# Kernel tuning notes

Measured on AMD Instinct MI355X. Metric: run time of the kernel, lower is better.

## Reference

```python
import jax, jax.numpy as jnp
import numpy as np

HEADS = 8
DIM_KEY = 32
DIM_VALUE = 32
SCALE = DIM_KEY ** -0.5
RED = 2  # reduction_factor


def _conv(x, w, stride):
    # NHWC input, HWIO kernel, VALID padding (keras Conv2D default)
    return jax.lax.conv_general_dilated(
        x, w, window_strides=(stride, stride), padding='VALID',
        dimension_numbers=('NHWC', 'HWIO', 'NHWC'))


def _split_heads(t, h):
    # [b, H, W, h*d] -> [b, h, H*W, d]
    b, H, W, hd = t.shape
    d = hd // h
    return t.reshape(b, H * W, h, d).transpose(0, 2, 1, 3)


def setup_inputs() -> dict:
    key = jax.random.key(0)
    ks = jax.random.split(key, 6)
    dim = 256
    x = jax.random.normal(ks[0], (8, 56, 56, dim), dtype=jnp.float32)
    Wq = jax.random.normal(ks[1], (1, 1, dim, DIM_KEY * HEADS), dtype=jnp.float32) * 0.02
    Wk = jax.random.normal(ks[2], (RED, RED, dim, DIM_KEY * HEADS), dtype=jnp.float32) * 0.02
    Wv = jax.random.normal(ks[3], (RED, RED, dim, DIM_VALUE * HEADS), dtype=jnp.float32) * 0.02
    Wo = jax.random.normal(ks[4], (1, 1, DIM_VALUE * HEADS, dim), dtype=jnp.float32) * 0.02
    bo = jnp.zeros((dim,), dtype=jnp.float32)
    return {"x": x, "Wq": Wq, "Wk": Wk, "Wv": Wv, "Wo": Wo, "bo": bo}


def reference(x, Wq, Wk, Wv, Wo, bo):
    b, H, W, _ = x.shape
    q = _split_heads(_conv(x, Wq, 1), HEADS)      # [b, h, H*W, dk]
    k = _split_heads(_conv(x, Wk, RED), HEADS)    # [b, h, (H/R)*(W/R), dk]
    v = _split_heads(_conv(x, Wv, RED), HEADS)    # [b, h, (H/R)*(W/R), dv]
    dots = jnp.einsum('bhnd,bhmd->bhnm', q, k) * SCALE
    attn = jax.nn.softmax(dots, axis=-1)
    out = jnp.einsum('bhnm,bhmd->bhnd', attn, v)  # [b, h, H*W, dv]
    out = out.transpose(0, 2, 1, 3).reshape(b, H, W, HEADS * DIM_VALUE)
    out = _conv(out, Wo, 1) + bo                  # 1x1 output projection (dropout rate 0)
    return out
```

## Files before the change

kernel.cpp:

```cpp
#include <hip/hip_runtime.h>
#include <cstdint>
#include <cstddef>

typedef __bf16 bf16_t;
typedef __bf16 bf16x8 __attribute__((ext_vector_type(8)));
typedef __bf16 bf16x4 __attribute__((ext_vector_type(4)));
typedef float  f32x4  __attribute__((ext_vector_type(4)));
typedef unsigned int u32x2 __attribute__((ext_vector_type(2)));
typedef unsigned int u32x4 __attribute__((ext_vector_type(4)));

#define MFMA16(a,b,c) __builtin_amdgcn_mfma_f32_16x16x32_bf16((a),(b),(c),0,0,0)

#if __has_builtin(__builtin_amdgcn_exp2f)
#define EXP2F(x) __builtin_amdgcn_exp2f(x)
#else
#define EXP2F(x) exp2f(x)
#endif

namespace {
constexpr int BATCH = 8;
constexpr int NQ    = 56 * 56;
constexpr int NKV   = 28 * 28;
constexpr int NKVP  = 800;
constexpr float QSCALE = 0.17677669529663687f * 1.44269504088896340f;

constexpr size_t XB_ELEMS = (size_t)BATCH * 56 * 56 * 256;
constexpr size_t Q_ELEMS  = (size_t)64 * NQ * 32;
constexpr size_t K_ELEMS  = (size_t)64 * NKVP * 32;
constexpr size_t VT_ELEMS = (size_t)64 * 32 * NKVP;

constexpr size_t XB_OFF  = 0;
constexpr size_t Q_OFF   = XB_OFF + XB_ELEMS * 2;
constexpr size_t K_OFF   = Q_OFF + Q_ELEMS * 2;
constexpr size_t VT_OFF  = K_OFF + K_ELEMS * 2;
constexpr size_t WQT_OFF = VT_OFF + VT_ELEMS * 2;
constexpr size_t WKT_OFF = WQT_OFF + (size_t)65536 * 2;
constexpr size_t WVT_OFF = WKT_OFF + (size_t)262144 * 2;
constexpr size_t WOT_OFF = WVT_OFF + (size_t)262144 * 2;
}

__device__ __forceinline__ void perm32swap(uint32_t& a, uint32_t& b) {
  asm volatile("s_nop 1\n\tv_permlane32_swap_b32 %0, %1\n\ts_nop 1"
               : "+v"(a), "+v"(b));
}


__global__ __launch_bounds__(256) void k_prep(const float* __restrict__ x,
                                              const float* __restrict__ Wq,
                                              const float* __restrict__ Wk,
                                              const float* __restrict__ Wv,
                                              const float* __restrict__ Wo,
                                              bf16_t* __restrict__ xb,
                                              bf16_t* __restrict__ Wqt,
                                              bf16_t* __restrict__ Wkt,
                                              bf16_t* __restrict__ Wvt,
                                              bf16_t* __restrict__ Wot,
                                              bf16_t* __restrict__ Kh,
                                              bf16_t* __restrict__ Vt) {
  const int bid = blockIdx.x;
  if (bid < 6272) {
    int i = bid * 256 + threadIdx.x;
    float4 v = ((const float4*)x)[i];
    bf16x4 o;
    o[0] = (bf16_t)v.x; o[1] = (bf16_t)v.y; o[2] = (bf16_t)v.z; o[3] = (bf16_t)v.w;
    ((bf16x4*)xb)[i] = o;
    return;
  }
  if (bid < 6432) {
    __shared__ float tile[64][65];
    const int wid = bid - 6272;
    const float* w; bf16_t* wt; int K; float scale = 1.f; int local;
    if (wid < 16)       { w = Wq; wt = Wqt; K = 256;  scale = QSCALE; local = wid; }
    else if (wid < 80)  { w = Wk; wt = Wkt; K = 1024; local = wid - 16; }
    else if (wid < 144) { w = Wv; wt = Wvt; K = 1024; local = wid - 80; }
    else                { w = Wo; wt = Wot; K = 256;  local = wid - 144; }
    const int tk = (local >> 2) * 64, tn = (local & 3) * 64;
    const int t = threadIdx.x;
#pragma unroll
    for (int i = 0; i < 16; ++i) {
      int e = t + i * 256, kk = e >> 6, nn = e & 63;
      tile[kk][nn] = w[(size_t)(tk + kk) * 256 + tn + nn];
    }
    __syncthreads();
#pragma unroll
    for (int i = 0; i < 16; ++i) {
      int e = t + i * 256, nn = e >> 6, kk = e & 63;
      wt[(size_t)(tn + nn) * K + tk + kk] = (bf16_t)(tile[kk][nn] * scale);
    }
    return;
  }
  const int pair = bid - 6432;
  bf16_t* kp = Kh + (size_t)pair * NKVP * 32 + (size_t)NKV * 32;
  for (int i = threadIdx.x; i < 512; i += 256) kp[i] = (bf16_t)0.f;
  bf16_t* vp = Vt + (size_t)pair * 32 * NKVP;
  for (int i = threadIdx.x; i < 512; i += 256) {
    int d = i >> 4, c = i & 15;
    vp[(size_t)d * NKVP + NKV + c] = (bf16_t)0.f;
  }
}


__global__ __launch_bounds__(512) void k_gemm_q(const bf16_t* __restrict__ A,
                                                const bf16_t* __restrict__ Wt,
                                                bf16_t* __restrict__ Qh) {
  __shared__ __align__(16) char Blds[64 * 512];
  const int t = threadIdx.x;
  const int lane = t & 63, wv = t >> 6;
  const int lq = lane & 15, grp = lane >> 4;
  const int w = (blockIdx.x & 7) * 98 + (blockIdx.x >> 3);
  const int m0 = (w >> 2) * 128 + wv * 16;
  const int n0 = (w & 3) * 64;

#pragma unroll
  for (int i = 0; i < 4; ++i) {
    int c = t + i * 512;
    int r = c >> 5, cb = (c & 31) << 4;
    bf16x8 v = *(const bf16x8*)(Wt + (size_t)(n0 + r) * 256 + (cb >> 1));
    *(bf16x8*)(Blds + r * 512 + (cb ^ ((r & 7) << 4))) = v;
  }
  __syncthreads();

  const bf16_t* Arow = A + (size_t)(m0 + lq) * 256 + grp * 8;
  f32x4 acc[4] = {};
#pragma unroll
  for (int kk = 0; kk < 8; ++kk) {
    bf16x8 af = *(const bf16x8*)(Arow + kk * 32);
#pragma unroll
    for (int nt = 0; nt < 4; ++nt) {
      const int r = nt * 16 + lq;
      bf16x8 bfr = *(const bf16x8*)(Blds + r * 512 + ((kk * 64 + grp * 16) ^ ((r & 7) << 4)));
      acc[nt] = MFMA16(af, bfr, acc[nt]);
    }
  }

  const int grow = m0 + grp * 4;
  const int b = grow / NQ, pos = grow - b * NQ;
#pragma unroll
  for (int nt = 0; nt < 4; ++nt) {
    const int n = n0 + nt * 16 + lq;
    const int h = n >> 5, d = n & 31;
    bf16_t* dst = Qh + ((size_t)(b * 8 + h) * NQ + pos) * 32 + d;
#pragma unroll
    for (int j = 0; j < 4; ++j) dst[(size_t)j * 32] = (bf16_t)acc[nt][j];
  }
}


__global__ __launch_bounds__(512) void k_gemm_kv(const bf16_t* __restrict__ xb,
                                                 const bf16_t* __restrict__ Wkt,
                                                 const bf16_t* __restrict__ Wvt,
                                                 bf16_t* __restrict__ Kh,
                                                 bf16_t* __restrict__ Vt) {
  __shared__ __align__(16) char Blds[64 * 1024];
  const int t = threadIdx.x;
  const int lane = t & 63, wv = t >> 6;
  const int lq = lane & 15, grp = lane >> 4;
  const int w = (blockIdx.x & 7) * 49 + (blockIdx.x >> 3);
  const int rem = w & 7;
  const int mode = rem & 1;
  const int n0 = (rem >> 1) * 64;
  const int mt = (w >> 3) * 128 + wv * 16;
  const bf16_t* Wt = mode ? Wvt : Wkt;

  const int grow = mt + lq;
  const int b = grow / NKV, pos = grow - b * NKV;
  const int pi = pos / 28, pj = pos % 28;
  const bf16_t* x4[4];
#pragma unroll
  for (int hw = 0; hw < 4; ++hw) {
    const int h_ = hw >> 1, w_ = hw & 1;
    x4[hw] = xb + ((size_t)((b * 56 + 2 * pi + h_) * 56) + 2 * pj + w_) * 256 + grp * 8;
  }

  f32x4 acc[4] = {};
#pragma unroll
  for (int half = 0; half < 2; ++half) {
    if (half) __syncthreads();
#pragma unroll
    for (int i = 0; i < 8; ++i) {
      int c = t + i * 512;
      int r = c >> 6, cb = (c & 63) << 4;
      bf16x8 v = *(const bf16x8*)(Wt + (size_t)(n0 + r) * 1024 + half * 512 + (cb >> 1));
      *(bf16x8*)(Blds + r * 1024 + (cb ^ ((r & 7) << 4))) = v;
    }
    __syncthreads();
#pragma unroll
    for (int kk = 0; kk < 16; ++kk) {
      const int gk = half * 16 + kk;
      const int hw = gk >> 3, kkk = gk & 7;
      bf16x8 af = *(const bf16x8*)(x4[hw] + kkk * 32);
#pragma unroll
      for (int nt = 0; nt < 4; ++nt) {
        const int r = nt * 16 + lq;
        bf16x8 bfr = *(const bf16x8*)(Blds + r * 1024 + ((kk * 64 + grp * 16) ^ ((r & 7) << 4)));
        acc[nt] = MFMA16(af, bfr, acc[nt]);
      }
    }
  }

  const int mbase = mt + grp * 4;
  const int b2 = mbase / NKV, pos2 = mbase - b2 * NKV;
  if (mode == 0) {
#pragma unroll
    for (int nt = 0; nt < 4; ++nt) {
      const int n = n0 + nt * 16 + lq;
      const int h = n >> 5, d = n & 31;
      bf16_t* dst = Kh + ((size_t)(b2 * 8 + h) * NKVP + pos2) * 32 + d;
#pragma unroll
      for (int j = 0; j < 4; ++j) dst[(size_t)j * 32] = (bf16_t)acc[nt][j];
    }
  } else {
#pragma unroll
    for (int nt = 0; nt < 4; ++nt) {
      const int n = n0 + nt * 16 + lq;
      const int h = n >> 5, d = n & 31;
      bf16x4 v;
#pragma unroll
      for (int j = 0; j < 4; ++j) v[j] = (bf16_t)acc[nt][j];
      *(bf16x4*)&Vt[((size_t)(b2 * 8 + h) * 32 + d) * NKVP + pos2] = v;
    }
  }
}


__global__ __launch_bounds__(256) void k_attn(const bf16_t* __restrict__ Qh,
                                              const bf16_t* __restrict__ Kh,
                                              const bf16_t* __restrict__ Vt,
                                              bf16_t* __restrict__ att) {
  const int lane = threadIdx.x & 63, wv = threadIdx.x >> 6;
  const int lq = lane & 15, grp = lane >> 4;
  const int wg = blockIdx.x;
  const int idx = wg >> 3;
  const int ygrp = (wg & 7) * 2 + idx / 98;
  const int pair = ygrp * 4 + wv;
  const int q0 = (idx % 98) * 32;

  const bf16_t* Qbase = Qh + ((size_t)pair * NQ + q0) * 32;
  bf16x8 qf[2];
#pragma unroll
  for (int t = 0; t < 2; ++t)
    qf[t] = *(const bf16x8*)(Qbase + (size_t)(t * 16 + lq) * 32 + grp * 8);

  const int prow = (lq & 3) | ((lq & 4) << 1) | ((lq & 8) >> 1);
  const bf16_t* Kb = Kh + (size_t)pair * NKVP * 32 + (size_t)prow * 32 + grp * 8;
  const bf16_t* Vb = Vt + (size_t)pair * 32 * NKVP + grp * 8;

  const f32x4 fz = {0.f, 0.f, 0.f, 0.f};
  f32x4 ps[2] = {fz, fz};
  f32x4 ot[2][2] = {{fz, fz}, {fz, fz}};

  bf16x8 Ak0, Ak1, Av0, Av1, Bk0, Bk1, Bv0, Bv1;

#define LOADF(P, CH) do { const int kv0_ = (CH) * 32;                          \
    P##k0 = *(const bf16x8*)(Kb + (size_t)kv0_ * 32);                          \
    P##k1 = *(const bf16x8*)(Kb + (size_t)(kv0_ + 16) * 32);                   \
    P##v0 = *(const bf16x8*)(Vb + (size_t)lq * NKVP + kv0_);                   \
    P##v1 = *(const bf16x8*)(Vb + (size_t)(16 + lq) * NKVP + kv0_); } while (0)

#define COMPUTE(P) do {                                                        \
    _Pragma("unroll")                                                          \
    for (int t = 0; t < 2; ++t) {                                              \
      f32x4 s0 = MFMA16(P##k0, qf[t], fz);                                     \
      f32x4 s1 = MFMA16(P##k1, qf[t], fz);                                     \
      f32x4 e0, e1;                                                            \
      _Pragma("unroll")                                                        \
      for (int j = 0; j < 4; ++j) { e0[j] = EXP2F(s0[j]); e1[j] = EXP2F(s1[j]); } \
      ps[t] += e0 + e1;                                                        \
      bf16x4 pa, pb;                                                           \
      _Pragma("unroll")                                                        \
      for (int j = 0; j < 4; ++j) { pa[j] = (bf16_t)e0[j]; pb[j] = (bf16_t)e1[j]; } \
      u32x2 ua = __builtin_bit_cast(u32x2, pa);                                \
      u32x2 ub = __builtin_bit_cast(u32x2, pb);                                \
      uint32_t x0 = ua[0], x1 = ua[1], y0 = ub[0], y1 = ub[1];                 \
      perm32swap(x0, y0);                                                      \
      perm32swap(x1, y1);                                                      \
      u32x4 pfu = {x0, x1, y0, y1};                                            \
      bf16x8 pf = __builtin_bit_cast(bf16x8, pfu);                             \
      ot[t][0] = MFMA16(P##v0, pf, ot[t][0]);                                  \
      ot[t][1] = MFMA16(P##v1, pf, ot[t][1]);                                  \
    } } while (0)

  LOADF(A, 0);
#pragma unroll 1
  for (int i = 0; i < 12; ++i) {
    LOADF(B, 2 * i + 1);
    COMPUTE(A);
    LOADF(A, 2 * i + 2);
    COMPUTE(B);
  }
  COMPUTE(A);
#undef LOADF
#undef COMPUTE

#pragma unroll
  for (int t = 0; t < 2; ++t) {
    float l = ps[t][0] + ps[t][1] + ps[t][2] + ps[t][3];
    l += __shfl_xor(l, 16, 64);
    l += __shfl_xor(l, 32, 64);
    const float inv = 1.f / (l - 16.f);
    bf16_t* obase = att + ((size_t)pair * NQ + q0 + t * 16 + lq) * 32;
    bf16x4 o0, o1;
#pragma unroll
    for (int j = 0; j < 4; ++j) {
      o0[j] = (bf16_t)(ot[t][0][j] * inv);
      o1[j] = (bf16_t)(ot[t][1][j] * inv);
    }
    *(bf16x4*)(obase + grp * 4) = o0;
    *(bf16x4*)(obase + 16 + grp * 4) = o1;
  }
}


__global__ __launch_bounds__(512) void k_gemm_proj(const bf16_t* __restrict__ A,
                                                   const bf16_t* __restrict__ Wt,
                                                   const float* __restrict__ bias,
                                                   float* __restrict__ out) {
  __shared__ __align__(16) char Blds[64 * 512];
  const int t = threadIdx.x;
  const int lane = t & 63, wv = t >> 6;
  const int lq = lane & 15, grp = lane >> 4;
  const int w = (blockIdx.x & 7) * 98 + (blockIdx.x >> 3);
  const int m0 = (w >> 2) * 128 + wv * 16;
  const int n0 = (w & 3) * 64;

#pragma unroll
  for (int i = 0; i < 4; ++i) {
    int c = t + i * 512;
    int r = c >> 5, cb = (c & 31) << 4;
    bf16x8 v = *(const bf16x8*)(Wt + (size_t)(n0 + r) * 256 + (cb >> 1));
    *(bf16x8*)(Blds + r * 512 + (cb ^ ((r & 7) << 4))) = v;
  }
  __syncthreads();

  const int gm = m0 + lq;
  const int b = gm / NQ, pos = gm - b * NQ;
  f32x4 acc[4] = {};
#pragma unroll
  for (int kk = 0; kk < 8; ++kk) {
    bf16x8 af = *(const bf16x8*)(A + ((size_t)(b * 8 + kk) * NQ + pos) * 32 + grp * 8);
#pragma unroll
    for (int nt = 0; nt < 4; ++nt) {
      const int r = nt * 16 + lq;
      bf16x8 bfr = *(const bf16x8*)(Blds + r * 512 + ((kk * 64 + grp * 16) ^ ((r & 7) << 4)));
      acc[nt] = MFMA16(af, bfr, acc[nt]);
    }
  }

  const int mrow = m0 + grp * 4;
#pragma unroll
  for (int nt = 0; nt < 4; ++nt) {
    const int nn = n0 + nt * 16 + lq;
    const float bb = bias[nn];
#pragma unroll
    for (int j = 0; j < 4; ++j)
      out[(size_t)(mrow + j) * 256 + nn] = acc[nt][j] + bb;
  }
}


extern "C" void kernel_launch(void* const* d_in, const int* in_sizes, int n_in,
                              void* d_out, int out_size, void* d_ws, size_t ws_size,
                              hipStream_t stream) {
  const float* x  = (const float*)d_in[0];
  const float* Wq = (const float*)d_in[1];
  const float* Wk = (const float*)d_in[2];
  const float* Wv = (const float*)d_in[3];
  const float* Wo = (const float*)d_in[4];
  const float* bo = (const float*)d_in[5];
  float* out = (float*)d_out;

  char* ws = (char*)d_ws;
  bf16_t* xb  = (bf16_t*)(ws + XB_OFF);
  bf16_t* Qh  = (bf16_t*)(ws + Q_OFF);
  bf16_t* att = Qh;
  bf16_t* Kh  = (bf16_t*)(ws + K_OFF);
  bf16_t* Vt  = (bf16_t*)(ws + VT_OFF);
  bf16_t* Wqt = (bf16_t*)(ws + WQT_OFF);
  bf16_t* Wkt = (bf16_t*)(ws + WKT_OFF);
  bf16_t* Wvt = (bf16_t*)(ws + WVT_OFF);
  bf16_t* Wot = (bf16_t*)(ws + WOT_OFF);

  k_prep<<<6496, 256, 0, stream>>>(x, Wq, Wk, Wv, Wo, xb, Wqt, Wkt, Wvt, Wot, Kh, Vt);
  k_gemm_q<<<784, 512, 0, stream>>>(xb, Wqt, Qh);
  k_gemm_kv<<<392, 512, 0, stream>>>(xb, Wkt, Wvt, Kh, Vt);
  k_attn<<<1568, 256, 0, stream>>>(Qh, Kh, Vt, att);
  k_gemm_proj<<<784, 512, 0, stream>>>(att, Wot, bo, out);
}
```

Measured before the change: 101.5 us.

## Merge Q and KV projection GEMMs into one launch; split attention accumulators

```diff
diff --git a/kernel.cpp b/kernel.cpp
--- a/kernel.cpp
+++ b/kernel.cpp
@@ -100,62 +100,60 @@
 }
 
 
-__global__ __launch_bounds__(512) void k_gemm_q(const bf16_t* __restrict__ A,
-                                                const bf16_t* __restrict__ Wt,
-                                                bf16_t* __restrict__ Qh) {
-  __shared__ __align__(16) char Blds[64 * 512];
-  const int t = threadIdx.x;
-  const int lane = t & 63, wv = t >> 6;
-  const int lq = lane & 15, grp = lane >> 4;
-  const int w = (blockIdx.x & 7) * 98 + (blockIdx.x >> 3);
-  const int m0 = (w >> 2) * 128 + wv * 16;
-  const int n0 = (w & 3) * 64;
-
-#pragma unroll
-  for (int i = 0; i < 4; ++i) {
-    int c = t + i * 512;
-    int r = c >> 5, cb = (c & 31) << 4;
-    bf16x8 v = *(const bf16x8*)(Wt + (size_t)(n0 + r) * 256 + (cb >> 1));
-    *(bf16x8*)(Blds + r * 512 + (cb ^ ((r & 7) << 4))) = v;
-  }
-  __syncthreads();
-
-  const bf16_t* Arow = A + (size_t)(m0 + lq) * 256 + grp * 8;
-  f32x4 acc[4] = {};
-#pragma unroll
-  for (int kk = 0; kk < 8; ++kk) {
-    bf16x8 af = *(const bf16x8*)(Arow + kk * 32);
-#pragma unroll
-    for (int nt = 0; nt < 4; ++nt) {
-      const int r = nt * 16 + lq;
-      bf16x8 bfr = *(const bf16x8*)(Blds + r * 512 + ((kk * 64 + grp * 16) ^ ((r & 7) << 4)));
-      acc[nt] = MFMA16(af, bfr, acc[nt]);
-    }
-  }
-
-  const int grow = m0 + grp * 4;
-  const int b = grow / NQ, pos = grow - b * NQ;
-#pragma unroll
-  for (int nt = 0; nt < 4; ++nt) {
-    const int n = n0 + nt * 16 + lq;
-    const int h = n >> 5, d = n & 31;
-    bf16_t* dst = Qh + ((size_t)(b * 8 + h) * NQ + pos) * 32 + d;
-#pragma unroll
-    for (int j = 0; j < 4; ++j) dst[(size_t)j * 32] = (bf16_t)acc[nt][j];
-  }
-}
-
-
-__global__ __launch_bounds__(512) void k_gemm_kv(const bf16_t* __restrict__ xb,
-                                                 const bf16_t* __restrict__ Wkt,
-                                                 const bf16_t* __restrict__ Wvt,
-                                                 bf16_t* __restrict__ Kh,
-                                                 bf16_t* __restrict__ Vt) {
+__global__ __launch_bounds__(512) void k_gemm_qkv(const bf16_t* __restrict__ xb,
+                                                  const bf16_t* __restrict__ Wqt,
+                                                  const bf16_t* __restrict__ Wkt,
+                                                  const bf16_t* __restrict__ Wvt,
+                                                  bf16_t* __restrict__ Qh,
+                                                  bf16_t* __restrict__ Kh,
+                                                  bf16_t* __restrict__ Vt) {
   __shared__ __align__(16) char Blds[64 * 1024];
   const int t = threadIdx.x;
   const int lane = t & 63, wv = t >> 6;
   const int lq = lane & 15, grp = lane >> 4;
-  const int w = (blockIdx.x & 7) * 49 + (blockIdx.x >> 3);
+
+  if (blockIdx.x < 784) {
+    const int w = ((int)blockIdx.x & 7) * 98 + ((int)blockIdx.x >> 3);
+    const int m0 = (w >> 2) * 128 + wv * 16;
+    const int n0 = (w & 3) * 64;
+
+#pragma unroll
+    for (int i = 0; i < 4; ++i) {
+      int c = t + i * 512;
+      int r = c >> 5, cb = (c & 31) << 4;
+      bf16x8 v = *(const bf16x8*)(Wqt + (size_t)(n0 + r) * 256 + (cb >> 1));
+      *(bf16x8*)(Blds + r * 512 + (cb ^ ((r & 7) << 4))) = v;
+    }
+    __syncthreads();
+
+    const bf16_t* Arow = xb + (size_t)(m0 + lq) * 256 + grp * 8;
+    f32x4 acc[4] = {};
+#pragma unroll
+    for (int kk = 0; kk < 8; ++kk) {
+      bf16x8 af = *(const bf16x8*)(Arow + kk * 32);
+#pragma unroll
+      for (int nt = 0; nt < 4; ++nt) {
+        const int r = nt * 16 + lq;
+        bf16x8 bfr = *(const bf16x8*)(Blds + r * 512 + ((kk * 64 + grp * 16) ^ ((r & 7) << 4)));
+        acc[nt] = MFMA16(af, bfr, acc[nt]);
+      }
+    }
+
+    const int grow = m0 + grp * 4;
+    const int b = grow / NQ, pos = grow - b * NQ;
+#pragma unroll
+    for (int nt = 0; nt < 4; ++nt) {
+      const int n = n0 + nt * 16 + lq;
+      const int h = n >> 5, d = n & 31;
+      bf16_t* dst = Qh + ((size_t)(b * 8 + h) * NQ + pos) * 32 + d;
+#pragma unroll
+      for (int j = 0; j < 4; ++j) dst[(size_t)j * 32] = (bf16_t)acc[nt][j];
+    }
+    return;
+  }
+
+  const int bid2 = (int)blockIdx.x - 784;
+  const int w = (bid2 & 7) * 49 + (bid2 >> 3);
   const int rem = w & 7;
   const int mode = rem & 1;
   const int n0 = (rem >> 1) * 64;
@@ -246,8 +244,9 @@
   const bf16_t* Vb = Vt + (size_t)pair * 32 * NKVP + grp * 8;
 
   const f32x4 fz = {0.f, 0.f, 0.f, 0.f};
-  f32x4 ps[2] = {fz, fz};
-  f32x4 ot[2][2] = {{fz, fz}, {fz, fz}};
+  f32x4 psA[2] = {fz, fz}, psB[2] = {fz, fz};
+  f32x4 otA[2][2] = {{fz, fz}, {fz, fz}};
+  f32x4 otB[2][2] = {{fz, fz}, {fz, fz}};
 
   bf16x8 Ak0, Ak1, Av0, Av1, Bk0, Bk1, Bv0, Bv1;
 
@@ -265,7 +264,7 @@
       f32x4 e0, e1;                                                            \
       _Pragma("unroll")                                                        \
       for (int j = 0; j < 4; ++j) { e0[j] = EXP2F(s0[j]); e1[j] = EXP2F(s1[j]); } \
-      ps[t] += e0 + e1;                                                        \
+      ps##P[t] += e0 + e1;                                                     \
       bf16x4 pa, pb;                                                           \
       _Pragma("unroll")                                                        \
       for (int j = 0; j < 4; ++j) { pa[j] = (bf16_t)e0[j]; pb[j] = (bf16_t)e1[j]; } \
@@ -276,8 +275,8 @@
       perm32swap(x1, y1);                                                      \
       u32x4 pfu = {x0, x1, y0, y1};                                            \
       bf16x8 pf = __builtin_bit_cast(bf16x8, pfu);                             \
-      ot[t][0] = MFMA16(P##v0, pf, ot[t][0]);                                  \
-      ot[t][1] = MFMA16(P##v1, pf, ot[t][1]);                                  \
+      ot##P[t][0] = MFMA16(P##v0, pf, ot##P[t][0]);                            \
+      ot##P[t][1] = MFMA16(P##v1, pf, ot##P[t][1]);                            \
     } } while (0)
 
   LOADF(A, 0);
@@ -294,16 +293,19 @@
 
 #pragma unroll
   for (int t = 0; t < 2; ++t) {
-    float l = ps[t][0] + ps[t][1] + ps[t][2] + ps[t][3];
+    f32x4 ps = psA[t] + psB[t];
+    float l = ps[0] + ps[1] + ps[2] + ps[3];
     l += __shfl_xor(l, 16, 64);
     l += __shfl_xor(l, 32, 64);
     const float inv = 1.f / (l - 16.f);
+    f32x4 o0f = otA[t][0] + otB[t][0];
+    f32x4 o1f = otA[t][1] + otB[t][1];
     bf16_t* obase = att + ((size_t)pair * NQ + q0 + t * 16 + lq) * 32;
     bf16x4 o0, o1;
 #pragma unroll
     for (int j = 0; j < 4; ++j) {
-      o0[j] = (bf16_t)(ot[t][0][j] * inv);
-      o1[j] = (bf16_t)(ot[t][1][j] * inv);
+      o0[j] = (bf16_t)(o0f[j] * inv);
+      o1[j] = (bf16_t)(o1f[j] * inv);
     }
     *(bf16x4*)(obase + grp * 4) = o0;
     *(bf16x4*)(obase + 16 + grp * 4) = o1;
@@ -381,8 +383,7 @@
   bf16_t* Wot = (bf16_t*)(ws + WOT_OFF);
 
   k_prep<<<6496, 256, 0, stream>>>(x, Wq, Wk, Wv, Wo, xb, Wqt, Wkt, Wvt, Wot, Kh, Vt);
-  k_gemm_q<<<784, 512, 0, stream>>>(xb, Wqt, Qh);
-  k_gemm_kv<<<392, 512, 0, stream>>>(xb, Wkt, Wvt, Kh, Vt);
+  k_gemm_qkv<<<1176, 512, 0, stream>>>(xb, Wqt, Wkt, Wvt, Qh, Kh, Vt);
   k_attn<<<1568, 256, 0, stream>>>(Qh, Kh, Vt, att);
   k_gemm_proj<<<784, 512, 0, stream>>>(att, Wot, bo, out);
 }
```

Result: no change. 100.7 us (-0.8%).
